# Performance work log

Measured on AMD Instinct MI355X. Metric: run time of the kernel, lower is better.

## Reference

```python
import jax, jax.numpy as jnp
import numpy as np

B, U, D = 256, 512, 512

def setup_inputs() -> dict:
    key = jax.random.key(0)
    ks = jax.random.split(key, 12)
    return {
        "x": jax.random.normal(ks[0], (B, D), jnp.float32),
        "h_tm1": jax.random.normal(ks[1], (B, U), jnp.float32) * 0.1,
        "c_tm1": jax.random.normal(ks[2], (B, U), jnp.float32) * 0.1,
        "hebb": jax.random.normal(ks[3], (B, U, U), jnp.float32) * 0.1,
        "kernel": jax.random.normal(ks[4], (D, 4 * U), jnp.float32) * (1.0 / np.sqrt(D)),
        "rec_kernel": jax.random.normal(ks[5], (U, 4 * U), jnp.float32) * (1.0 / np.sqrt(U)),
        "bias": jax.random.normal(ks[6], (4 * U,), jnp.float32) * 0.01,
        "w": 0.02 * jax.random.uniform(ks[7], (U, U), jnp.float32) - 0.01,
        "alpha": 0.0001 * jax.random.uniform(ks[8], (1, 1, U), jnp.float32),
        "h2mod": jax.random.normal(ks[9], (U, 1), jnp.float32) * (1.0 / np.sqrt(U)),
        "fanout": jax.random.normal(ks[10], (1, U), jnp.float32),
    }

def reference(x, h_tm1, c_tm1, hebb, kernel, rec_kernel, bias, w, alpha, h2mod, fanout):
    U_ = w.shape[0]
    hard_sigmoid = lambda z: jnp.clip(0.2 * z + 0.5, 0.0, 1.0)  # keras hard_sigmoid
    gx = x @ kernel + bias                      # [B,4U]
    x_i, x_f, x_c, x_o = jnp.split(gx, 4, axis=-1)
    i = hard_sigmoid(x_i + h_tm1 @ rec_kernel[:, :U_])
    f = hard_sigmoid(x_f + h_tm1 @ rec_kernel[:, U_:2 * U_])
    o = hard_sigmoid(x_o + h_tm1 @ rec_kernel[:, 3 * U_:])
    # plastic recurrent path: per-sample fast weights (w + alpha*hebb)
    h2c = jnp.einsum('bu,buv->bv', h_tm1, w + alpha * hebb)  # [B,U]
    inputstocell = jnp.tanh(x_c + h2c)
    c = f * c_tm1 + i * inputstocell
    h = o * jnp.tanh(c)
    # rank-1 hebbian update, neuromodulated eta
    deltahebb = h_tm1[:, :, None] * inputstocell[:, None, :]  # [B,U,U]
    myeta = jnp.tanh(h @ h2mod)                 # [B,1]
    myeta = (myeta @ fanout)[:, None, :]        # [B,1,U]
    hebb_new = jnp.clip(hebb + myeta * deltahebb, -2.0, 2.0)
    return h, c, hebb_new
```

## Files before the change

kernel.cpp:

```cpp
#include <hip/hip_runtime.h>

#define B_ 256
#define U_ 512
#define NG 2048

__device__ __forceinline__ float hsig(float z) {
    return fminf(fmaxf(0.2f * z + 0.5f, 0.f), 1.f);
}

__global__ __launch_bounds__(256) void gemm_preact(
    const float* __restrict__ x, const float* __restrict__ h,
    const float* __restrict__ kern, const float* __restrict__ reck,
    const float* __restrict__ w, const float* __restrict__ bias,
    float* __restrict__ preact)
{
    __shared__ float As[64][20];
    __shared__ float Bs[16][64];
    const int tid = threadIdx.x;
    const int tx = tid & 15, ty = tid >> 4;
    const int m0 = blockIdx.y * 64;
    const int n0 = blockIdx.x * 64;
    float acc[4][4] = {};

    for (int phase = 0; phase < 2; ++phase) {
        const float* A = phase ? h : x;
        const float* Bp;
        int bstride;
        if (phase == 0)                { Bp = kern + n0;          bstride = NG; }
        else if (n0 >= 2*U_ && n0 < 3*U_) { Bp = w + (n0 - 2*U_); bstride = U_; }
        else                           { Bp = reck + n0;          bstride = NG; }

        for (int k0 = 0; k0 < 512; k0 += 16) {
            {
                const int row = tid >> 2;
                const int kk  = (tid & 3) * 4;
                float4 a4 = *(const float4*)(A + (size_t)(m0 + row) * 512 + k0 + kk);
                *(float4*)&As[row][kk] = a4;
            }
            {
                const int kk  = tid >> 4;
                const int col = (tid & 15) * 4;
                float4 b4 = *(const float4*)(Bp + (size_t)(k0 + kk) * bstride + col);
                *(float4*)&Bs[kk][col] = b4;
            }
            __syncthreads();
            #pragma unroll
            for (int kk = 0; kk < 16; ++kk) {
                float a0 = As[ty*4+0][kk], a1 = As[ty*4+1][kk];
                float a2 = As[ty*4+2][kk], a3 = As[ty*4+3][kk];
                float b0 = Bs[kk][tx*4+0], b1 = Bs[kk][tx*4+1];
                float b2 = Bs[kk][tx*4+2], b3 = Bs[kk][tx*4+3];
                acc[0][0] = fmaf(a0,b0,acc[0][0]); acc[0][1] = fmaf(a0,b1,acc[0][1]);
                acc[0][2] = fmaf(a0,b2,acc[0][2]); acc[0][3] = fmaf(a0,b3,acc[0][3]);
                acc[1][0] = fmaf(a1,b0,acc[1][0]); acc[1][1] = fmaf(a1,b1,acc[1][1]);
                acc[1][2] = fmaf(a1,b2,acc[1][2]); acc[1][3] = fmaf(a1,b3,acc[1][3]);
                acc[2][0] = fmaf(a2,b0,acc[2][0]); acc[2][1] = fmaf(a2,b1,acc[2][1]);
                acc[2][2] = fmaf(a2,b2,acc[2][2]); acc[2][3] = fmaf(a2,b3,acc[2][3]);
                acc[3][0] = fmaf(a3,b0,acc[3][0]); acc[3][1] = fmaf(a3,b1,acc[3][1]);
                acc[3][2] = fmaf(a3,b2,acc[3][2]); acc[3][3] = fmaf(a3,b3,acc[3][3]);
            }
            __syncthreads();
        }
    }
    #pragma unroll
    for (int i = 0; i < 4; ++i) {
        const int row = m0 + ty*4 + i;
        const int col = n0 + tx*4;
        float4 o;
        o.x = acc[i][0] + bias[col+0];
        o.y = acc[i][1] + bias[col+1];
        o.z = acc[i][2] + bias[col+2];
        o.w = acc[i][3] + bias[col+3];
        *(float4*)(preact + (size_t)row * NG + col) = o;
    }
}

__global__ __launch_bounds__(256) void hebb_reduce(
    const float* __restrict__ hebb, const float* __restrict__ h_tm1,
    float* __restrict__ hebbsum)
{
    const int b   = blockIdx.x;
    const int us  = blockIdx.y;
    const int tid = threadIdx.x;
    const int vl  = tid & 127;
    const int ug  = tid >> 7;
    const int v   = vl * 4;

    __shared__ float hsh[128];
    if (tid < 128) hsh[tid] = h_tm1[b * 512 + us * 128 + tid];
    __syncthreads();

    const float* hb = hebb + ((size_t)b * 512 + us * 128 + ug) * 512 + v;
    float4 acc = make_float4(0.f, 0.f, 0.f, 0.f);
    #pragma unroll 4
    for (int i = 0; i < 64; ++i) {
        const float hs = hsh[i * 2 + ug];
        float4 hv = *(const float4*)(hb + (size_t)i * 1024);
        acc.x = fmaf(hs, hv.x, acc.x);
        acc.y = fmaf(hs, hv.y, acc.y);
        acc.z = fmaf(hs, hv.z, acc.z);
        acc.w = fmaf(hs, hv.w, acc.w);
    }

    __shared__ float4 red[128];
    if (ug) red[vl] = acc;
    __syncthreads();
    if (!ug) {
        float4 o = red[vl];
        float* dst = hebbsum + b * 512 + v;
        atomicAdd(dst + 0, acc.x + o.x);
        atomicAdd(dst + 1, acc.y + o.y);
        atomicAdd(dst + 2, acc.z + o.z);
        atomicAdd(dst + 3, acc.w + o.w);
    }
}

__global__ __launch_bounds__(512) void cell_kernel(
    const float* __restrict__ preact, const float* __restrict__ hebbsum,
    const float* __restrict__ alpha, const float* __restrict__ c_tm1,
    const float* __restrict__ h2mod,
    float* __restrict__ out_h, float* __restrict__ out_c,
    float* __restrict__ itc_ws, float* __restrict__ etab_ws)
{
    const int b = blockIdx.x;
    const int v = threadIdx.x;
    const float* pr = preact + (size_t)b * NG;
    const float pi = pr[v], pf = pr[512 + v], pc = pr[1024 + v], po = pr[1536 + v];

    const float h2c = fmaf(alpha[v], hebbsum[b * 512 + v], pc);
    const float itc = tanhf(h2c);
    const float gi = hsig(pi), gf = hsig(pf), go = hsig(po);
    const float c  = gf * c_tm1[b * 512 + v] + gi * itc;
    const float hh = go * tanhf(c);

    out_h[b * 512 + v]  = hh;
    out_c[b * 512 + v]  = c;
    itc_ws[b * 512 + v] = itc;

    float d = hh * h2mod[v];
    #pragma unroll
    for (int off = 32; off > 0; off >>= 1) d += __shfl_down(d, off, 64);
    __shared__ float wred[8];
    if ((v & 63) == 0) wred[v >> 6] = d;
    __syncthreads();
    if (v == 0) {
        float s = 0.f;
        #pragma unroll
        for (int k = 0; k < 8; ++k) s += wred[k];
        etab_ws[b] = tanhf(s);
    }
}

__global__ __launch_bounds__(256) void hebb_update(
    const float* __restrict__ hebb, const float* __restrict__ h_tm1,
    const float* __restrict__ itc_ws, const float* __restrict__ fanout,
    const float* __restrict__ etab_ws, float* __restrict__ out_hebb)
{
    const int b   = blockIdx.x;
    const int us  = blockIdx.y;
    const int tid = threadIdx.x;
    const int vl  = tid & 127;
    const int ug  = tid >> 7;
    const int v   = vl * 4;

    __shared__ float hsh[128];
    if (tid < 128) hsh[tid] = h_tm1[b * 512 + us * 128 + tid];
    __syncthreads();

    const float eta = etab_ws[b];
    float4 fv = *(const float4*)(fanout + v);
    float4 iv = *(const float4*)(itc_ws + b * 512 + v);
    float4 ef;
    ef.x = eta * fv.x * iv.x; ef.y = eta * fv.y * iv.y;
    ef.z = eta * fv.z * iv.z; ef.w = eta * fv.w * iv.w;

    const size_t base = ((size_t)b * 512 + us * 128 + ug) * 512 + v;
    #pragma unroll 4
    for (int i = 0; i < 64; ++i) {
        const float hs = hsh[i * 2 + ug];
        float4 hv = *(const float4*)(hebb + base + (size_t)i * 1024);
        float4 o;
        o.x = fminf(fmaxf(fmaf(ef.x, hs, hv.x), -2.f), 2.f);
        o.y = fminf(fmaxf(fmaf(ef.y, hs, hv.y), -2.f), 2.f);
        o.z = fminf(fmaxf(fmaf(ef.z, hs, hv.z), -2.f), 2.f);
        o.w = fminf(fmaxf(fmaf(ef.w, hs, hv.w), -2.f), 2.f);
        *(float4*)(out_hebb + base + (size_t)i * 1024) = o;
    }
}

extern "C" void kernel_launch(void* const* d_in, const int* in_sizes, int n_in,
                              void* d_out, int out_size, void* d_ws, size_t ws_size,
                              hipStream_t stream)
{
    const float* x      = (const float*)d_in[0];
    const float* h_tm1  = (const float*)d_in[1];
    const float* c_tm1  = (const float*)d_in[2];
    const float* hebb   = (const float*)d_in[3];
    const float* kern   = (const float*)d_in[4];
    const float* reck   = (const float*)d_in[5];
    const float* bias   = (const float*)d_in[6];
    const float* w      = (const float*)d_in[7];
    const float* alpha  = (const float*)d_in[8];
    const float* h2mod  = (const float*)d_in[9];
    const float* fanout = (const float*)d_in[10];

    float* out_h    = (float*)d_out;
    float* out_c    = out_h + (size_t)B_ * U_;
    float* out_hebb = out_c + (size_t)B_ * U_;

    float* ws       = (float*)d_ws;
    float* hebbsum  = ws;
    float* itc      = ws + (size_t)B_ * U_;
    float* etab     = ws + (size_t)2 * B_ * U_;
    float* preact   = ws + (size_t)2 * B_ * U_ + 256;

    hipMemsetAsync(hebbsum, 0, (size_t)B_ * U_ * sizeof(float), stream);
    gemm_preact<<<dim3(32, 4), 256, 0, stream>>>(x, h_tm1, kern, reck, w, bias, preact);
    hebb_reduce<<<dim3(256, 4), 256, 0, stream>>>(hebb, h_tm1, hebbsum);
    cell_kernel<<<256, 512, 0, stream>>>(preact, hebbsum, alpha, c_tm1, h2mod,
                                         out_h, out_c, itc, etab);
    hebb_update<<<dim3(256, 4), 256, 0, stream>>>(hebb, h_tm1, itc, fanout, etab, out_hebb);
}
```

Before: 639.3 us.

## Fuse GEMM with hebb reduction and merge cell math into hebb update

Runs the gate GEMM and the hebb-weighted reduction as two block groups of one launch, so the small GEMM overlaps with the bandwidth-bound reduction. The reduction now writes per-slice partial sums instead of using atomics, which removes the memset. The cell computation is folded into the hebb update kernel: each of the four slice blocks per sample recomputes the cell and eta redundantly. This drops two launches and the itc/eta workspace round trips, at the cost of 4x redundant cell math and extra partial-sum traffic. The GEMM's A tile is also stored transposed so it can be read with float4 loads.

```diff
diff --git a/kernel.cpp b/kernel.cpp
--- a/kernel.cpp
+++ b/kernel.cpp
@@ -8,174 +8,173 @@
     return fminf(fmaxf(0.2f * z + 0.5f, 0.f), 1.f);
 }
 
-__global__ __launch_bounds__(256) void gemm_preact(
+__global__ __launch_bounds__(256) void fused_gemm_reduce(
     const float* __restrict__ x, const float* __restrict__ h,
     const float* __restrict__ kern, const float* __restrict__ reck,
     const float* __restrict__ w, const float* __restrict__ bias,
-    float* __restrict__ preact)
+    const float* __restrict__ hebb,
+    float* __restrict__ preact, float* __restrict__ partial)
 {
-    __shared__ float As[64][20];
-    __shared__ float Bs[16][64];
     const int tid = threadIdx.x;
-    const int tx = tid & 15, ty = tid >> 4;
-    const int m0 = blockIdx.y * 64;
-    const int n0 = blockIdx.x * 64;
-    float acc[4][4] = {};
-
-    for (int phase = 0; phase < 2; ++phase) {
-        const float* A = phase ? h : x;
-        const float* Bp;
-        int bstride;
-        if (phase == 0)                { Bp = kern + n0;          bstride = NG; }
-        else if (n0 >= 2*U_ && n0 < 3*U_) { Bp = w + (n0 - 2*U_); bstride = U_; }
-        else                           { Bp = reck + n0;          bstride = NG; }
-
-        for (int k0 = 0; k0 < 512; k0 += 16) {
-            {
-                const int row = tid >> 2;
-                const int kk  = (tid & 3) * 4;
-                float4 a4 = *(const float4*)(A + (size_t)(m0 + row) * 512 + k0 + kk);
-                *(float4*)&As[row][kk] = a4;
+
+    if (blockIdx.x < 128) {
+        __shared__ float As[16][68];
+        __shared__ float Bs[16][68];
+        const int gb = blockIdx.x;
+        const int n0 = (gb & 31) * 64;
+        const int m0 = (gb >> 5) * 64;
+        const int tx = tid & 15, ty = tid >> 4;
+        float acc[4][4] = {};
+
+        for (int phase = 0; phase < 2; ++phase) {
+            const float* A = phase ? h : x;
+            const float* Bp;
+            int bstride;
+            if (phase == 0)                     { Bp = kern + n0;         bstride = NG; }
+            else if (n0 >= 2*U_ && n0 < 3*U_)   { Bp = w + (n0 - 2*U_);   bstride = U_; }
+            else                                { Bp = reck + n0;         bstride = NG; }
+
+            for (int k0 = 0; k0 < 512; k0 += 16) {
+                {
+                    const int row = tid >> 2;
+                    const int kq  = (tid & 3) * 4;
+                    float4 a4 = *(const float4*)(A + (size_t)(m0 + row) * 512 + k0 + kq);
+                    As[kq+0][row] = a4.x; As[kq+1][row] = a4.y;
+                    As[kq+2][row] = a4.z; As[kq+3][row] = a4.w;
+                }
+                {
+                    const int kk  = tid >> 4;
+                    const int col = (tid & 15) * 4;
+                    float4 b4 = *(const float4*)(Bp + (size_t)(k0 + kk) * bstride + col);
+                    *(float4*)&Bs[kk][col] = b4;
+                }
+                __syncthreads();
+                #pragma unroll
+                for (int kk = 0; kk < 16; ++kk) {
+                    float4 a4 = *(const float4*)&As[kk][ty*4];
+                    float4 b4 = *(const float4*)&Bs[kk][tx*4];
+                    const float a[4] = {a4.x, a4.y, a4.z, a4.w};
+                    const float b[4] = {b4.x, b4.y, b4.z, b4.w};
+                    #pragma unroll
+                    for (int i = 0; i < 4; ++i) {
+                        acc[i][0] = fmaf(a[i], b[0], acc[i][0]);
+                        acc[i][1] = fmaf(a[i], b[1], acc[i][1]);
+                        acc[i][2] = fmaf(a[i], b[2], acc[i][2]);
+                        acc[i][3] = fmaf(a[i], b[3], acc[i][3]);
+                    }
+                }
+                __syncthreads();
             }
-            {
-                const int kk  = tid >> 4;
-                const int col = (tid & 15) * 4;
-                float4 b4 = *(const float4*)(Bp + (size_t)(k0 + kk) * bstride + col);
-                *(float4*)&Bs[kk][col] = b4;
-            }
-            __syncthreads();
-            #pragma unroll
-            for (int kk = 0; kk < 16; ++kk) {
-                float a0 = As[ty*4+0][kk], a1 = As[ty*4+1][kk];
-                float a2 = As[ty*4+2][kk], a3 = As[ty*4+3][kk];
-                float b0 = Bs[kk][tx*4+0], b1 = Bs[kk][tx*4+1];
-                float b2 = Bs[kk][tx*4+2], b3 = Bs[kk][tx*4+3];
-                acc[0][0] = fmaf(a0,b0,acc[0][0]); acc[0][1] = fmaf(a0,b1,acc[0][1]);
-                acc[0][2] = fmaf(a0,b2,acc[0][2]); acc[0][3] = fmaf(a0,b3,acc[0][3]);
-                acc[1][0] = fmaf(a1,b0,acc[1][0]); acc[1][1] = fmaf(a1,b1,acc[1][1]);
-                acc[1][2] = fmaf(a1,b2,acc[1][2]); acc[1][3] = fmaf(a1,b3,acc[1][3]);
-                acc[2][0] = fmaf(a2,b0,acc[2][0]); acc[2][1] = fmaf(a2,b1,acc[2][1]);
-                acc[2][2] = fmaf(a2,b2,acc[2][2]); acc[2][3] = fmaf(a2,b3,acc[2][3]);
-                acc[3][0] = fmaf(a3,b0,acc[3][0]); acc[3][1] = fmaf(a3,b1,acc[3][1]);
-                acc[3][2] = fmaf(a3,b2,acc[3][2]); acc[3][3] = fmaf(a3,b3,acc[3][3]);
-            }
-            __syncthreads();
+        }
+        #pragma unroll
+        for (int i = 0; i < 4; ++i) {
+            const int row = m0 + ty*4 + i;
+            const int col = n0 + tx*4;
+            float4 o;
+            o.x = acc[i][0] + bias[col+0];
+            o.y = acc[i][1] + bias[col+1];
+            o.z = acc[i][2] + bias[col+2];
+            o.w = acc[i][3] + bias[col+3];
+            *(float4*)(preact + (size_t)row * NG + col) = o;
+        }
+    } else {
+        __shared__ float  hsh[128];
+        __shared__ float4 red[128];
+        const int rid = blockIdx.x - 128;
+        const int b   = rid >> 2;
+        const int us  = rid & 3;
+        const int vl  = tid & 127;
+        const int ug  = tid >> 7;
+        const int v   = vl * 4;
+
+        if (tid < 128) hsh[tid] = h[b * 512 + us * 128 + tid];
+        __syncthreads();
+
+        const float* hb = hebb + ((size_t)b * 512 + us * 128 + ug) * 512 + v;
+        float4 acc = make_float4(0.f, 0.f, 0.f, 0.f);
+        #pragma unroll 8
+        for (int i = 0; i < 64; ++i) {
+            const float hs = hsh[i * 2 + ug];
+            float4 hv = *(const float4*)(hb + (size_t)i * 1024);
+            acc.x = fmaf(hs, hv.x, acc.x);
+            acc.y = fmaf(hs, hv.y, acc.y);
+            acc.z = fmaf(hs, hv.z, acc.z);
+            acc.w = fmaf(hs, hv.w, acc.w);
+        }
+
+        if (ug) red[vl] = acc;
+        __syncthreads();
+        if (!ug) {
+            float4 o = red[vl];
+            o.x += acc.x; o.y += acc.y; o.z += acc.z; o.w += acc.w;
+            *(float4*)(partial + ((size_t)us * 256 + b) * 512 + v) = o;
         }
     }
-    #pragma unroll
-    for (int i = 0; i < 4; ++i) {
-        const int row = m0 + ty*4 + i;
-        const int col = n0 + tx*4;
-        float4 o;
-        o.x = acc[i][0] + bias[col+0];
-        o.y = acc[i][1] + bias[col+1];
-        o.z = acc[i][2] + bias[col+2];
-        o.w = acc[i][3] + bias[col+3];
-        *(float4*)(preact + (size_t)row * NG + col) = o;
-    }
-}
-
-__global__ __launch_bounds__(256) void hebb_reduce(
-    const float* __restrict__ hebb, const float* __restrict__ h_tm1,
-    float* __restrict__ hebbsum)
+}
+
+__global__ __launch_bounds__(256) void cell_update(
+    const float* __restrict__ preact, const float* __restrict__ partial,
+    const float* __restrict__ alpha, const float* __restrict__ c_tm1,
+    const float* __restrict__ h_tm1, const float* __restrict__ h2mod,
+    const float* __restrict__ fanout, const float* __restrict__ hebb,
+    float* __restrict__ out_h, float* __restrict__ out_c,
+    float* __restrict__ out_hebb)
 {
     const int b   = blockIdx.x;
     const int us  = blockIdx.y;
     const int tid = threadIdx.x;
-    const int vl  = tid & 127;
-    const int ug  = tid >> 7;
-    const int v   = vl * 4;
-
+
+    __shared__ float itc_sh[512];
     __shared__ float hsh[128];
+    __shared__ float wred[4];
+    __shared__ float eta_sh;
+
+    const float* pr = preact + (size_t)b * NG;
+    float hv2[2];
+    #pragma unroll
+    for (int s = 0; s < 2; ++s) {
+        const int v = tid + s * 256;
+        const float hsum = partial[(0*256 + b) * 512 + v]
+                         + partial[(1*256 + b) * 512 + v]
+                         + partial[(2*256 + b) * 512 + v]
+                         + partial[(3*256 + b) * 512 + v];
+        const float itc = tanhf(fmaf(alpha[v], hsum, pr[1024 + v]));
+        const float gi = hsig(pr[v]);
+        const float gf = hsig(pr[512 + v]);
+        const float go = hsig(pr[1536 + v]);
+        const float c  = gf * c_tm1[b * 512 + v] + gi * itc;
+        const float hh = go * tanhf(c);
+        itc_sh[v] = itc;
+        hv2[s] = hh;
+        if (us == 0) {
+            out_h[b * 512 + v] = hh;
+            out_c[b * 512 + v] = c;
+        }
+    }
     if (tid < 128) hsh[tid] = h_tm1[b * 512 + us * 128 + tid];
-    __syncthreads();
-
-    const float* hb = hebb + ((size_t)b * 512 + us * 128 + ug) * 512 + v;
-    float4 acc = make_float4(0.f, 0.f, 0.f, 0.f);
-    #pragma unroll 4
-    for (int i = 0; i < 64; ++i) {
-        const float hs = hsh[i * 2 + ug];
-        float4 hv = *(const float4*)(hb + (size_t)i * 1024);
-        acc.x = fmaf(hs, hv.x, acc.x);
-        acc.y = fmaf(hs, hv.y, acc.y);
-        acc.z = fmaf(hs, hv.z, acc.z);
-        acc.w = fmaf(hs, hv.w, acc.w);
-    }
-
-    __shared__ float4 red[128];
-    if (ug) red[vl] = acc;
-    __syncthreads();
-    if (!ug) {
-        float4 o = red[vl];
-        float* dst = hebbsum + b * 512 + v;
-        atomicAdd(dst + 0, acc.x + o.x);
-        atomicAdd(dst + 1, acc.y + o.y);
-        atomicAdd(dst + 2, acc.z + o.z);
-        atomicAdd(dst + 3, acc.w + o.w);
-    }
-}
-
-__global__ __launch_bounds__(512) void cell_kernel(
-    const float* __restrict__ preact, const float* __restrict__ hebbsum,
-    const float* __restrict__ alpha, const float* __restrict__ c_tm1,
-    const float* __restrict__ h2mod,
-    float* __restrict__ out_h, float* __restrict__ out_c,
-    float* __restrict__ itc_ws, float* __restrict__ etab_ws)
-{
-    const int b = blockIdx.x;
-    const int v = threadIdx.x;
-    const float* pr = preact + (size_t)b * NG;
-    const float pi = pr[v], pf = pr[512 + v], pc = pr[1024 + v], po = pr[1536 + v];
-
-    const float h2c = fmaf(alpha[v], hebbsum[b * 512 + v], pc);
-    const float itc = tanhf(h2c);
-    const float gi = hsig(pi), gf = hsig(pf), go = hsig(po);
-    const float c  = gf * c_tm1[b * 512 + v] + gi * itc;
-    const float hh = go * tanhf(c);
-
-    out_h[b * 512 + v]  = hh;
-    out_c[b * 512 + v]  = c;
-    itc_ws[b * 512 + v] = itc;
-
-    float d = hh * h2mod[v];
+
+    float d = hv2[0] * h2mod[tid] + hv2[1] * h2mod[tid + 256];
     #pragma unroll
     for (int off = 32; off > 0; off >>= 1) d += __shfl_down(d, off, 64);
-    __shared__ float wred[8];
-    if ((v & 63) == 0) wred[v >> 6] = d;
+    if ((tid & 63) == 0) wred[tid >> 6] = d;
     __syncthreads();
-    if (v == 0) {
-        float s = 0.f;
-        #pragma unroll
-        for (int k = 0; k < 8; ++k) s += wred[k];
-        etab_ws[b] = tanhf(s);
-    }
-}
-
-__global__ __launch_bounds__(256) void hebb_update(
-    const float* __restrict__ hebb, const float* __restrict__ h_tm1,
-    const float* __restrict__ itc_ws, const float* __restrict__ fanout,
-    const float* __restrict__ etab_ws, float* __restrict__ out_hebb)
-{
-    const int b   = blockIdx.x;
-    const int us  = blockIdx.y;
-    const int tid = threadIdx.x;
-    const int vl  = tid & 127;
-    const int ug  = tid >> 7;
-    const int v   = vl * 4;
-
-    __shared__ float hsh[128];
-    if (tid < 128) hsh[tid] = h_tm1[b * 512 + us * 128 + tid];
+    if (tid == 0) eta_sh = tanhf(wred[0] + wred[1] + wred[2] + wred[3]);
     __syncthreads();
-
-    const float eta = etab_ws[b];
+    const float eta = eta_sh;
+
+    const int vl = tid & 127;
+    const int ug = tid >> 7;
+    const int v  = vl * 4;
+
     float4 fv = *(const float4*)(fanout + v);
-    float4 iv = *(const float4*)(itc_ws + b * 512 + v);
     float4 ef;
-    ef.x = eta * fv.x * iv.x; ef.y = eta * fv.y * iv.y;
-    ef.z = eta * fv.z * iv.z; ef.w = eta * fv.w * iv.w;
+    ef.x = eta * fv.x * itc_sh[v + 0];
+    ef.y = eta * fv.y * itc_sh[v + 1];
+    ef.z = eta * fv.z * itc_sh[v + 2];
+    ef.w = eta * fv.w * itc_sh[v + 3];
 
     const size_t base = ((size_t)b * 512 + us * 128 + ug) * 512 + v;
-    #pragma unroll 4
+    #pragma unroll 8
     for (int i = 0; i < 64; ++i) {
         const float hs = hsh[i * 2 + ug];
         float4 hv = *(const float4*)(hebb + base + (size_t)i * 1024);
@@ -208,16 +207,13 @@
     float* out_c    = out_h + (size_t)B_ * U_;
     float* out_hebb = out_c + (size_t)B_ * U_;
 
-    float* ws       = (float*)d_ws;
-    float* hebbsum  = ws;
-    float* itc      = ws + (size_t)B_ * U_;
-    float* etab     = ws + (size_t)2 * B_ * U_;
-    float* preact   = ws + (size_t)2 * B_ * U_ + 256;
-
-    hipMemsetAsync(hebbsum, 0, (size_t)B_ * U_ * sizeof(float), stream);
-    gemm_preact<<<dim3(32, 4), 256, 0, stream>>>(x, h_tm1, kern, reck, w, bias, preact);
-    hebb_reduce<<<dim3(256, 4), 256, 0, stream>>>(hebb, h_tm1, hebbsum);
-    cell_kernel<<<256, 512, 0, stream>>>(preact, hebbsum, alpha, c_tm1, h2mod,
-                                         out_h, out_c, itc, etab);
-    hebb_update<<<dim3(256, 4), 256, 0, stream>>>(hebb, h_tm1, itc, fanout, etab, out_hebb);
-}
+    float* ws      = (float*)d_ws;
+    float* partial = ws;
+    float* preact  = ws + (size_t)4 * B_ * U_;
+
+    fused_gemm_reduce<<<128 + 1024, 256, 0, stream>>>(
+        x, h_tm1, kern, reck, w, bias, hebb, preact, partial);
+    cell_update<<<dim3(256, 4), 256, 0, stream>>>(
+        preact, partial, alpha, c_tm1, h_tm1, h2mod, fanout, hebb,
+        out_h, out_c, out_hebb);
+}
```

New measurement: 597.0 us. 6.6% less time.
